# Kernel tuning notes

Measured on AMD Instinct MI355X. Metric: run time of the kernel, lower is better.

Reference implementation:

```python
import jax, jax.numpy as jnp
import numpy as np

B, T, N, D = 4, 24, 5000, 64
M, K = 256, 20
TEMP = 0.5
MASK_T = int(T * 0.2)


def _random_walk(A):
    # D^-1 A with inf -> 0, as in calculate_random_walk_matrix
    deg = A.sum(axis=1)
    d_inv = jnp.where(deg > 0, 1.0 / deg, 0.0)
    return d_inv[:, None] * A


def _gnn(h, S1, S2, W, b):
    # SpatialConvOrderK, order=1, support_len=2, include_self=True
    # h: [B, C, N, T]; diffusion along node axis; 1x1 conv == channel matmul
    m1 = jnp.einsum('bcnt,mn->bcmt', h, S1)
    m2 = jnp.einsum('bcnt,mn->bcmt', h, S2)
    hc = jnp.concatenate([h, m1, m2], axis=1)  # [B, 3C, N, T]
    return jnp.einsum('bcnt,cd->bdnt', hc, W) + b[None, :, None, None]


def _encode(x, S1, S2, W_start, b_start, W1, b1, W2, b2):
    h = x @ W_start + b_start                 # [B, T, N, D]
    h = jnp.transpose(h, (0, 3, 2, 1))        # [B, D, N, T]
    h = jax.nn.relu(_gnn(h, S1, S2, W1, b1))
    h = _gnn(h, S1, S2, W2, b2)
    return h                                  # [B, D, N, T]


def _normalize(z):
    # cosine-similarity normalization over channel axis (dim=1), torch eps=1e-8
    n = jnp.sqrt(jnp.sum(z * z, axis=1, keepdims=True))
    return z / jnp.maximum(n, 1e-8)


def _forward(x, adj, W_start, b_start, W1, b1, W2, b2, Wf1, bf1, Wf2, bf2,
             missing_idx, pos_idx, neg_idx):
    S1 = _random_walk(adj)
    S2 = _random_walk(adj.T)
    h_ori = _encode(x, S1, S2, W_start, b_start, W1, b1, W2, b2)
    # augmented view: time-masked input through the same encoder
    x_aug = x.at[:, :MASK_T].set(0.0)
    h_aug = _encode(x_aug, S1, S2, W_start, b_start, W1, b1, W2, b2)
    # imputation head: final_linear1 -> relu -> final_linear2
    ht = jnp.transpose(h_ori, (0, 3, 2, 1))   # [B, T, N, D]
    y = jax.nn.relu(ht @ Wf1 + bf1) @ Wf2 + bf2  # [B, T, N, 1]
    # vectorized RSCL: batched gather + cosine sim + InfoNCE (label 0 = positive)
    Zo = _normalize(jnp.transpose(h_ori, (0, 1, 3, 2)))  # [B, D, T, N]
    Za = _normalize(jnp.transpose(h_aug, (0, 1, 3, 2)))
    anchor = Zo[..., missing_idx]             # [B, D, T, M]
    pos = Za[..., pos_idx]                    # [B, D, T, M]
    neg = Za[..., neg_idx]                    # [B, D, T, M, K]
    pos_sim = jnp.sum(anchor * pos, axis=1)                  # [B, T, M]
    neg_sim = jnp.einsum('bdtm,bdtmk->btmk', anchor, neg)    # [B, T, M, K]
    logits = jnp.concatenate([pos_sim[..., None], neg_sim], axis=-1) / TEMP
    # cross-entropy with label 0 == logsumexp - positive logit
    loss = jnp.mean(jax.nn.logsumexp(logits, axis=-1) - logits[..., 0])
    return y, loss


def setup_inputs() -> dict:
    key = jax.random.key(0)
    ks = jax.random.split(key, 12)
    x = jax.random.normal(ks[0], (B, T, N, 1), jnp.float32)
    adj = jax.random.uniform(ks[1], (N, N), jnp.float32)
    missing_idx = jax.random.randint(ks[2], (M,), 0, N)
    pos_idx = jax.random.randint(ks[3], (M,), 0, N)
    neg_idx = jax.random.randint(ks[4], (M, K), 0, N)
    s = lambda k, shp, fan: (jax.random.normal(k, shp, jnp.float32) / np.sqrt(fan)).astype(jnp.float32)
    W_start = s(ks[5], (1, D), 1.0)
    b_start = jnp.zeros((D,), jnp.float32)
    W1 = s(ks[6], (3 * D, D), 3.0 * D)
    b1 = jnp.zeros((D,), jnp.float32)
    W2 = s(ks[7], (3 * D, D), 3.0 * D)
    b2 = jnp.zeros((D,), jnp.float32)
    Wf1 = s(ks[8], (D, D // 2), float(D))
    bf1 = jnp.zeros((D // 2,), jnp.float32)
    Wf2 = s(ks[9], (D // 2, 1), float(D // 2))
    bf2 = jnp.zeros((1,), jnp.float32)
    return dict(x=x, adj=adj, W_start=W_start, b_start=b_start, W1=W1, b1=b1,
                W2=W2, b2=b2, Wf1=Wf1, bf1=bf1, Wf2=Wf2, bf2=bf2,
                missing_idx=missing_idx, pos_idx=pos_idx, neg_idx=neg_idx)


def reference(x, adj, W_start, b_start, W1, b1, W2, b2, Wf1, bf1, Wf2, bf2,
              missing_idx, pos_idx, neg_idx):
    return _forward(x, adj, W_start, b_start, W1, b1, W2, b2, Wf1, bf1, Wf2, bf2,
                    missing_idx, pos_idx, neg_idx)
```

## Files before the change

kernel.cpp:

```cpp
#include <hip/hip_runtime.h>

typedef unsigned char u8;
typedef unsigned short u16;
typedef unsigned int u32;
typedef __attribute__((ext_vector_type(8))) short short8;
typedef __attribute__((ext_vector_type(8))) u16 u16x8;
typedef __attribute__((ext_vector_type(4))) float f32x4;
typedef __attribute__((ext_vector_type(4))) int i32x4;
typedef __attribute__((ext_vector_type(8))) int i32x8;

#define N_NODES 5000
#define NP 5120
#define BTOT 96
#define J_DIM 6144
#define TT 24
#define KNEG 20

__device__ __forceinline__ float b2f(u16 u){ union{u32 i; float f;} x; x.i = ((u32)u)<<16; return x.f; }
__device__ __forceinline__ u16 f2b(float f){ union{float fl; u32 i;} x; x.fl = f; u32 r = (x.i + 0x7fffu + ((x.i>>16)&1u))>>16; return (u16)r; }
__device__ __forceinline__ u8 f2e4(float f){ return (u8)(__builtin_amdgcn_cvt_pk_fp8_f32(f, 0.f, 0, false) & 0xff); }

#define GPERM(r) ((((r)>>1)&3) | (((r)&1)<<2))
#define GLOAD16(g, l) __builtin_amdgcn_global_load_lds((const __attribute__((address_space(1))) void*)(g), (__attribute__((address_space(3))) void*)(l), 16, 0, 0)

__global__ void k_prep(const float* __restrict__ Ws, const float* __restrict__ bs,
                       const float* __restrict__ W1, const float* __restrict__ b1,
                       const float* __restrict__ W2, float* __restrict__ consts,
                       u16* __restrict__ w2t)
{
  int d = threadIdx.x;
  float u0=0.f,u1=0.f,u2=0.f,bb=0.f;
  for (int c=0;c<64;c++){
    float w = Ws[c];
    float a = W1[c*64+d], b_ = W1[(64+c)*64+d], cw = W1[(128+c)*64+d];
    u0 += w*a; u1 += w*b_; u2 += w*cw;
    bb += bs[c]*(a+b_+cw);
  }
  bb += b1[d];
  consts[d]=u0; consts[64+d]=u1; consts[128+d]=u2; consts[192+d]=bb;
  __shared__ float rb[64];
  rb[d] = fmaxf(bb, 0.f);
  __syncthreads();
  float cA=0.f,cB=0.f,cC=0.f;
  for (int c=0;c<64;c++){
    float r = rb[c];
    cA += r*W2[c*64+d]; cB += r*W2[(64+c)*64+d]; cC += r*W2[(128+c)*64+d];
  }
  consts[256+d]=cA; consts[320+d]=cB; consts[384+d]=cC;
  for (int c=0;c<192;c++) w2t[d*192 + c] = f2b(W2[c*64 + d]);
}

__global__ __launch_bounds__(256) void k_convT(const float* __restrict__ adj,
    u8* __restrict__ abf, u8* __restrict__ atbf,
    float* __restrict__ degr, float* __restrict__ degc)
{
  __shared__ u8 tN[64][80];
  __shared__ u8 tT[64][80];
  __shared__ float rsum[64], csum[64];
  const int tid = threadIdx.x;
  const int bx = blockIdx.x, by = blockIdx.y;
  if (tid < 64){ rsum[tid] = 0.f; csum[tid] = 0.f; }
  __syncthreads();
  const int c4 = (tid & 15) * 4;
  const int r0 = tid >> 4;
  const int gk = bx*64 + c4;
  float ca0=0.f, ca1=0.f, ca2=0.f, ca3=0.f;
  #pragma unroll
  for (int p=0;p<4;p++){
    int r = p*16 + r0;
    int gm = by*64 + r;
    float v0=0.f,v1=0.f,v2=0.f,v3=0.f;
    if (gm < N_NODES && gk + 3 < N_NODES){
      const float4 v = *(const float4*)(adj + (size_t)gm*N_NODES + gk);
      v0=v.x; v1=v.y; v2=v.z; v3=v.w;
    }
    u8 p0=f2e4(v0), p1=f2e4(v1), p2=f2e4(v2), p3=f2e4(v3);
    *(u32*)&tN[r][c4] = (u32)p0 | ((u32)p1<<8) | ((u32)p2<<16) | ((u32)p3<<24);
    tT[c4+0][r]=p0; tT[c4+1][r]=p1; tT[c4+2][r]=p2; tT[c4+3][r]=p3;
    float ls = v0+v1+v2+v3;
    if (ls != 0.f) atomicAdd(&rsum[r], ls);
    ca0+=v0; ca1+=v1; ca2+=v2; ca3+=v3;
  }
  atomicAdd(&csum[c4+0], ca0); atomicAdd(&csum[c4+1], ca1);
  atomicAdd(&csum[c4+2], ca2); atomicAdd(&csum[c4+3], ca3);
  __syncthreads();
  if (tid < 64){
    int gm = by*64 + tid;
    if (gm < N_NODES && rsum[tid] != 0.f) atomicAdd(&degr[gm], rsum[tid]);
    int gc = bx*64 + tid;
    if (gc < N_NODES && csum[tid] != 0.f) atomicAdd(&degc[gc], csum[tid]);
  }
  const int j = tid >> 2, c16 = (tid & 3) * 16;
  *(i32x4*)(abf  + (size_t)(by*64+j)*NP + bx*64 + c16) = *(const i32x4*)(&tN[j][c16]);
  *(i32x4*)(atbf + (size_t)(bx*64+j)*NP + by*64 + c16) = *(const i32x4*)(&tT[j][c16]);
}

__global__ void k_xbf(const float* __restrict__ x, u8* __restrict__ xbf){
  int i4 = (blockIdx.x*256 + threadIdx.x)*4;
  int j = i4 / NP, n = i4 - j*NP;
  u32 w = 0;
  if (j < BTOT){
    #pragma unroll
    for (int e=0;e<4;e++){
      float v = (n+e < N_NODES) ? x[(size_t)j*N_NODES + n + e] : 0.f;
      w |= ((u32)f2e4(v)) << (8*e);
    }
  }
  *(u32*)(xbf + i4) = w;
}

__device__ __forceinline__ i32x8 frag8(const u8* lds, int row, int kb2){
  int g = GPERM(row & 7);
  int ba = row*128 + ((kb2 ^ g)<<4);
  union { i32x8 v; i32x4 h[2]; } f;
  f.h[0] = *(const i32x4*)(lds + ba);
  f.h[1] = *(const i32x4*)(lds + (ba^16));
  return f.v;
}

__global__ __launch_bounds__(256) void k_sgemm8(const u8* __restrict__ abf,
    const u8* __restrict__ atbf, const u8* __restrict__ B,
    float* __restrict__ y1sl, float* __restrict__ y2sl)
{
  __shared__ __align__(16) u8 lA[128*128];
  __shared__ __align__(16) u8 lB[128*128];
  const u8* A = blockIdx.z ? atbf : abf;
  float* ysl = blockIdx.z ? y2sl : y1sl;
  const int tid = threadIdx.x, lane = tid & 63, wv = tid >> 6;
  const int wm = (wv >> 1) * 64, wj = (wv & 1) * 64;
  const int m0 = blockIdx.x * 128;
  const int kbase = blockIdx.y * 640;
  f32x4 acc[4][4] = {};
  const int q = tid >> 3;
  const int sc = ((tid & 7) ^ GPERM(q & 7)) << 4;
  const u8* gA = A + (size_t)(m0 + q)*NP + kbase + sc;
  const u8* gB = B + (size_t)q*NP + kbase + sc;
  for (int k0 = 0; k0 < 640; k0 += 128) {
    #pragma unroll
    for (int s=0;s<4;s++){
      GLOAD16(gA + (size_t)(s*32)*NP + k0, (char*)lA + s*4096 + wv*1024);
      GLOAD16(gB + (size_t)(s*32)*NP + k0, (char*)lB + s*4096 + wv*1024);
    }
    __syncthreads();
    i32x8 af[4], bfv[4];
    const int kb2 = (lane >> 4) * 2;
    #pragma unroll
    for (int i=0;i<4;i++){
      af[i]  = frag8(lA, wm + i*16 + (lane&15), kb2);
      bfv[i] = frag8(lB, wj + i*16 + (lane&15), kb2);
    }
    #pragma unroll
    for (int i=0;i<4;i++)
      #pragma unroll
      for (int j=0;j<4;j++)
        acc[i][j] = __builtin_amdgcn_mfma_scale_f32_16x16x128_f8f6f4(
            af[i], bfv[j], acc[i][j], 0, 0, 0, 0x7f7f7f7f, 0, 0x7f7f7f7f);
    __syncthreads();
  }
  float* yb = ysl + (size_t)blockIdx.y * NP * 128;
  #pragma unroll
  for (int i=0;i<4;i++)
    #pragma unroll
    for (int r=0;r<4;r++){
      int row = m0 + wm + i*16 + (lane>>4)*4 + r;
      #pragma unroll
      for (int j=0;j<4;j++){
        int col = wj + j*16 + (lane&15);
        yb[(size_t)row*128 + col] = acc[i][j][r];
      }
    }
}

__global__ __launch_bounds__(256) void k_yred(const float* __restrict__ y1sl,
    const float* __restrict__ y2sl, const float* __restrict__ degr,
    const float* __restrict__ degc, float* __restrict__ y1r, float* __restrict__ y2r)
{
  __shared__ float tb[128][66];
  const int n0 = blockIdx.x*64;
  const int bt = threadIdx.x & 127, nh = threadIdx.x >> 7;
  const int nl = threadIdx.x & 63, bh = threadIdx.x >> 6;
  #pragma unroll 4
  for (int k=0;k<32;k++){
    int n = nh*32 + k;
    float s = 0.f;
    #pragma unroll
    for (int sl=0; sl<8; sl++) s += y1sl[((size_t)sl*NP + n0+n)*128 + bt];
    tb[bt][n] = s;
  }
  __syncthreads();
  {
    float dv = degr[n0+nl];
    float iv = (dv > 0.f) ? 1.f/dv : 0.f;
    #pragma unroll 4
    for (int b=0;b<32;b++){
      int btw = bh*32 + b;
      y1r[(size_t)btw*NP + n0 + nl] = iv * tb[btw][nl];
    }
  }
  __syncthreads();
  #pragma unroll 4
  for (int k=0;k<32;k++){
    int n = nh*32 + k;
    float s = 0.f;
    #pragma unroll
    for (int sl=0; sl<8; sl++) s += y2sl[((size_t)sl*NP + n0+n)*128 + bt];
    tb[bt][n] = s;
  }
  __syncthreads();
  {
    float dv = degc[n0+nl];
    float iv = (dv > 0.f) ? 1.f/dv : 0.f;
    #pragma unroll 4
    for (int b=0;b<32;b++){
      int btw = bh*32 + b;
      y2r[(size_t)btw*NP + n0 + nl] = iv * tb[btw][nl];
    }
  }
}

__global__ __launch_bounds__(256) void k_h1(const float* __restrict__ x,
    const float* __restrict__ y1r, const float* __restrict__ y2r,
    const float* __restrict__ consts, u8* __restrict__ h1t, u16* __restrict__ h1n)
{
  __shared__ u8 trT[64][80];
  const int tid = threadIdx.x;
  const int n = tid & 63, d0 = (tid >> 6) * 16;
  const int n0 = blockIdx.x * 64;
  const int bt = blockIdx.y;
  const int gn = n0 + n;
  const bool valid = gn < N_NODES;
  float xv  = valid ? x[(size_t)bt*N_NODES + gn] : 0.f;
  float y1s = y1r[(size_t)bt*NP + gn];
  float y2s = y2r[(size_t)bt*NP + gn];
  float hv[16];
  #pragma unroll
  for (int e=0;e<16;e++){
    int d = d0 + e;
    float v = 0.f;
    if (valid)
      v = fmaxf(xv*consts[d] + y1s*consts[64+d] + y2s*consts[128+d] + consts[192+d], 0.f);
    hv[e] = v;
    trT[d][n] = f2e4(v);
  }
  u16x8 p0, p1;
  #pragma unroll
  for (int e=0;e<8;e++){ p0[e]=f2b(hv[e]); p1[e]=f2b(hv[8+e]); }
  u16* dst = h1n + (size_t)gn*J_DIM + bt*64 + d0;
  *(u16x8*)dst = p0;
  *(u16x8*)(dst+8) = p1;
  __syncthreads();
  const int d = tid >> 2, c16 = (tid & 3) * 16;
  *(i32x4*)(h1t + (size_t)(bt*64+d)*NP + n0 + c16) = *(const i32x4*)(&trT[d][c16]);
}

__global__ __launch_bounds__(256) void k_gemm8(
    const u8* __restrict__ abf, const u8* __restrict__ atbf,
    const u8* __restrict__ Bt, u16* __restrict__ Pb, u16* __restrict__ Qb,
    const float* __restrict__ degr, const float* __restrict__ degc)
{
  __shared__ __align__(16) u8 lA[128*128];
  __shared__ __align__(16) u8 lB[128*128];
  const u8* A = blockIdx.z ? atbf : abf;
  u16* C = blockIdx.z ? Qb : Pb;
  const float* dg = blockIdx.z ? degc : degr;
  const int tid = threadIdx.x, lane = tid & 63, wv = tid >> 6;
  const int wm = (wv >> 1) * 64, wj = (wv & 1) * 64;
  const int m0 = blockIdx.x * 128;
  const int j0 = blockIdx.y * 128;
  f32x4 acc[4][4] = {};
  const int q = tid >> 3;
  const int sc = ((tid & 7) ^ GPERM(q & 7)) << 4;
  const u8* gA = A + (size_t)(m0 + q)*NP + sc;
  const u8* gB = Bt + (size_t)(j0 + q)*NP + sc;
  for (int k0 = 0; k0 < NP; k0 += 128) {
    #pragma unroll
    for (int s=0;s<4;s++){
      GLOAD16(gA + (size_t)(s*32)*NP + k0, (char*)lA + s*4096 + wv*1024);
      GLOAD16(gB + (size_t)(s*32)*NP + k0, (char*)lB + s*4096 + wv*1024);
    }
    __syncthreads();
    i32x8 af[4], bfv[4];
    const int kb2 = (lane >> 4) * 2;
    #pragma unroll
    for (int i=0;i<4;i++){
      af[i]  = frag8(lA, wm + i*16 + (lane&15), kb2);
      bfv[i] = frag8(lB, wj + i*16 + (lane&15), kb2);
    }
    #pragma unroll
    for (int i=0;i<4;i++)
      #pragma unroll
      for (int j=0;j<4;j++)
        acc[i][j] = __builtin_amdgcn_mfma_scale_f32_16x16x128_f8f6f4(
            af[i], bfv[j], acc[i][j], 0, 0, 0, 0x7f7f7f7f, 0, 0x7f7f7f7f);
    __syncthreads();
  }
  #pragma unroll
  for (int i=0;i<4;i++)
    #pragma unroll
    for (int r=0;r<4;r++){
      int row = m0 + wm + i*16 + (lane>>4)*4 + r;
      float dv = dg[row];
      float scl = (dv > 0.f) ? 1.f/dv : 0.f;
      #pragma unroll
      for (int j=0;j<4;j++){
        int col = j0 + wj + j*16 + (lane&15);
        C[(size_t)row*J_DIM + col] = f2b(acc[i][j][r] * scl);
      }
    }
}

__global__ __launch_bounds__(256) void k_comb(const u16* __restrict__ h1n,
  const u16* __restrict__ P, const u16* __restrict__ Q,
  const u16* __restrict__ w2t, const float* __restrict__ b2,
  const float* __restrict__ Wf1, const float* __restrict__ bf1,
  const float* __restrict__ Wf2, const float* __restrict__ bf2,
  u16* __restrict__ hori, float* __restrict__ yout)
{
  __shared__ float w1L[64*33];
  __shared__ float hT[64][65];
  __shared__ float b1L[32], w2Ls[32];
  const int tid = threadIdx.x;
  for (int i = tid; i < 2048; i += 256) w1L[(i>>5)*33 + (i&31)] = Wf1[i];
  if (tid < 32){ b1L[tid] = bf1[tid]; w2Ls[tid] = Wf2[tid]; }
  const int lane = tid & 63;
  const int wv = tid >> 6;
  const int n0 = blockIdx.x * 64 + wv * 16;
  const int bt = blockIdx.y;
  const int rl = lane & 15, kh = lane >> 4;

  f32x4 acc[4] = {};
  const size_t rowoff = (size_t)(n0 + rl) * J_DIM + bt*64;
  const u16* bases[3] = { h1n + rowoff, P + rowoff, Q + rowoff };
  #pragma unroll
  for (int s=0;s<3;s++){
    const u16* base = bases[s];
    #pragma unroll
    for (int kk=0;kk<2;kk++){
      short8 af = *(const short8*)(base + kk*32 + kh*8);
      #pragma unroll
      for (int j=0;j<4;j++){
        short8 bf = *(const short8*)(w2t + (j*16+rl)*192 + s*64 + kk*32 + kh*8);
        acc[j] = __builtin_amdgcn_mfma_f32_16x16x32_bf16(af, bf, acc[j], 0,0,0);
      }
    }
  }
  #pragma unroll
  for (int j=0;j<4;j++){
    int d = j*16 + rl;
    float bias = b2[d];
    #pragma unroll
    for (int r=0;r<4;r++){
      float hv = acc[j][r] + bias;
      int nn = n0 + kh*4 + r;
      hT[wv*16 + kh*4 + r][d] = hv;
      if (nn < N_NODES)
        hori[((size_t)bt*N_NODES + nn)*64 + d] = f2b(hv);
    }
  }
  __syncthreads();
  const int q = tid & 3, node = tid >> 2;
  float h[16];
  #pragma unroll
  for (int e=0;e<16;e++) h[e] = hT[node][q*16 + e];
  float yacc = 0.f;
  #pragma unroll
  for (int jj=0; jj<32; jj++){
    float s = 0.f;
    #pragma unroll
    for (int dl=0; dl<16; dl++) s += h[dl]*w1L[(q*16+dl)*33 + jj];
    s += __shfl_xor(s, 1);
    s += __shfl_xor(s, 2);
    s += b1L[jj];
    yacc += fmaxf(s, 0.f)*w2Ls[jj];
  }
  int gn = blockIdx.x*64 + node;
  if (q == 0 && gn < N_NODES)
    yout[(size_t)bt*N_NODES + gn] = yacc + bf2[0];
}

__global__ __launch_bounds__(256) void k_loss(const u16* __restrict__ hori,
  const int* __restrict__ missing, const int* __restrict__ posi, const int* __restrict__ negi,
  const float* __restrict__ degr, const float* __restrict__ degc,
  const float* __restrict__ consts, const float* __restrict__ b2, float* __restrict__ out)
{
  const int lane = threadIdx.x & 63;
  const int wv = threadIdx.x >> 6;
  const int wg = blockIdx.x*4 + wv;
  const int m = wg & 255;
  const int bt = wg >> 8;
  const int t_ = bt % TT;
  const float cAv = consts[256+lane], cBv = consts[320+lane], cCv = consts[384+lane], b2v = b2[lane];

  int na = missing[m];
  float va = b2f(hori[((size_t)bt*N_NODES + na)*64 + lane]);
  float ss = va*va;
  #pragma unroll
  for (int o=32;o;o>>=1) ss += __shfl_xor(ss, o);
  va /= fmaxf(sqrtf(ss), 1e-8f);

  float l0 = 0.f, mx, se;
  {
    int node = posi[m];
    float v;
    if (t_ >= 4) v = b2f(hori[((size_t)bt*N_NODES + node)*64 + lane]);
    else {
      float r1 = (degr[node] > 0.f) ? 1.f : 0.f;
      float r2 = (degc[node] > 0.f) ? 1.f : 0.f;
      v = cAv + r1*cBv + r2*cCv + b2v;
    }
    float s2 = v*v;
    #pragma unroll
    for (int o=32;o;o>>=1) s2 += __shfl_xor(s2, o);
    v /= fmaxf(sqrtf(s2), 1e-8f);
    float dp = va*v;
    #pragma unroll
    for (int o=32;o;o>>=1) dp += __shfl_xor(dp, o);
    l0 = dp * 2.f;
  }
  mx = l0; se = 1.f;
  for (int k=0;k<KNEG;k++){
    int node = negi[m*KNEG + k];
    float v;
    if (t_ >= 4) v = b2f(hori[((size_t)bt*N_NODES + node)*64 + lane]);
    else {
      float r1 = (degr[node] > 0.f) ? 1.f : 0.f;
      float r2 = (degc[node] > 0.f) ? 1.f : 0.f;
      v = cAv + r1*cBv + r2*cCv + b2v;
    }
    float s2 = v*v;
    #pragma unroll
    for (int o=32;o;o>>=1) s2 += __shfl_xor(s2, o);
    v /= fmaxf(sqrtf(s2), 1e-8f);
    float dp = va*v;
    #pragma unroll
    for (int o=32;o;o>>=1) dp += __shfl_xor(dp, o);
    float lk = dp * 2.f;
    if (lk > mx){ se = se*expf(mx-lk) + 1.f; mx = lk; }
    else se += expf(lk-mx);
  }
  float term = logf(se) + mx - l0;
  __shared__ float red[4];
  if (lane == 0) red[wv] = term;
  __syncthreads();
  if (threadIdx.x == 0)
    atomicAdd(out + 480000, (red[0]+red[1]+red[2]+red[3]) * (1.f/24576.f));
}

extern "C" void kernel_launch(void* const* d_in, const int* in_sizes, int n_in,
                              void* d_out, int out_size, void* d_ws, size_t ws_size,
                              hipStream_t stream)
{
  const float* x   = (const float*)d_in[0];
  const float* adj = (const float*)d_in[1];
  const float* Ws  = (const float*)d_in[2];
  const float* bs  = (const float*)d_in[3];
  const float* W1  = (const float*)d_in[4];
  const float* b1  = (const float*)d_in[5];
  const float* W2  = (const float*)d_in[6];
  const float* b2  = (const float*)d_in[7];
  const float* Wf1 = (const float*)d_in[8];
  const float* bf1 = (const float*)d_in[9];
  const float* Wf2 = (const float*)d_in[10];
  const float* bf2 = (const float*)d_in[11];
  const int* missing = (const int*)d_in[12];
  const int* posi    = (const int*)d_in[13];
  const int* negi    = (const int*)d_in[14];
  float* out = (float*)d_out;

  char* w = (char*)d_ws;
  u8*  abf   = (u8*) (w + 0);
  u8*  atbf  = (u8*) (w + 26214400);
  u8*  h1t   = (u8*) (w + 52428800);
  u16* h1n   = (u16*)(w + 83886080);
  u16* Pb    = (u16*)(w + 146800640);
  u16* Qb    = (u16*)(w + 209715200);
  u8*  xbf   = (u8*) (w + 272629760);
  float* degr = (float*)(w + 273285120);
  float* degc = (float*)(w + 273305600);
  float* consts = (float*)(w + 273326080);
  u16* w2t   = (u16*)(w + 273328128);
  u16*   hori  = (u16*)(w + 0);
  float* y1sl  = (float*)(w + 146800640);
  float* y2sl  = (float*)(w + 167772160);
  float* y1r   = (float*)(w + 209715200);
  float* y2r   = (float*)(w + 212336640);

  hipMemsetAsync(degr, 0, 40960, stream);
  hipMemsetAsync(out + 480000, 0, 4, stream);

  k_prep<<<1, 64, 0, stream>>>(Ws, bs, W1, b1, W2, consts, w2t);
  k_convT<<<dim3(80,80), 256, 0, stream>>>(adj, abf, atbf, degr, degc);
  k_xbf<<<640, 256, 0, stream>>>(x, xbf);
  k_sgemm8<<<dim3(40,8,2), 256, 0, stream>>>(abf, atbf, xbf, y1sl, y2sl);
  k_yred<<<80, 256, 0, stream>>>(y1sl, y2sl, degr, degc, y1r, y2r);
  k_h1<<<dim3(80,96), 256, 0, stream>>>(x, y1r, y2r, consts, h1t, h1n);
  k_gemm8<<<dim3(40,48,2), 256, 0, stream>>>(abf, atbf, h1t, Pb, Qb, degr, degc);
  k_comb<<<dim3(80,96), 256, 0, stream>>>(h1n, Pb, Qb, w2t, b2, Wf1, bf1, Wf2, bf2, hori, out);
  k_loss<<<6144, 256, 0, stream>>>(hori, missing, posi, negi, degr, degc, consts, b2, out);
}
```

Measured before the change: 819.2 us.

## Pre-normalize embeddings in combine kernel and simplify loss and degree reductions

The combine kernel now L2-normalizes each node embedding before storing it. The loss kernel therefore only does dot products and no longer computes a per-gather norm. For early masked timesteps the four possible constant vectors are pre-normalized in the prep kernel. The loss uses unrolled independent gathers with a two-pass logsumexp, and the adjacency conversion replaces LDS atomics with shuffle and partial-sum reductions. Storing normalized bf16 values changes rounding slightly, and the larger unrolled loss kernel may raise register use.

```diff
diff --git a/kernel.cpp b/kernel.cpp
--- a/kernel.cpp
+++ b/kernel.cpp
@@ -25,8 +25,8 @@
 
 __global__ void k_prep(const float* __restrict__ Ws, const float* __restrict__ bs,
                        const float* __restrict__ W1, const float* __restrict__ b1,
-                       const float* __restrict__ W2, float* __restrict__ consts,
-                       u16* __restrict__ w2t)
+                       const float* __restrict__ W2, const float* __restrict__ b2,
+                       float* __restrict__ consts, u16* __restrict__ w2t)
 {
   int d = threadIdx.x;
   float u0=0.f,u1=0.f,u2=0.f,bb=0.f;
@@ -48,6 +48,17 @@
   }
   consts[256+d]=cA; consts[320+d]=cB; consts[384+d]=cC;
   for (int c=0;c<192;c++) w2t[d*192 + c] = f2b(W2[c*64 + d]);
+  __syncthreads();
+  float b2v = b2[d];
+  for (int vi=0; vi<4; vi++){
+    float vv = cA + ((vi&1) ? cB : 0.f) + ((vi&2) ? cC : 0.f) + b2v;
+    rb[d] = vv*vv;
+    __syncthreads();
+    for (int o=32;o;o>>=1){ if (d<o) rb[d]+=rb[d+o]; __syncthreads(); }
+    float nrm = sqrtf(rb[0]);
+    consts[448 + vi*64 + d] = vv / fmaxf(nrm, 1e-8f);
+    __syncthreads();
+  }
 }
 
 __global__ __launch_bounds__(256) void k_convT(const float* __restrict__ adj,
@@ -56,18 +67,17 @@
 {
   __shared__ u8 tN[64][80];
   __shared__ u8 tT[64][80];
-  __shared__ float rsum[64], csum[64];
+  __shared__ float rsum[64];
+  __shared__ float cpart[16][64];
   const int tid = threadIdx.x;
   const int bx = blockIdx.x, by = blockIdx.y;
-  if (tid < 64){ rsum[tid] = 0.f; csum[tid] = 0.f; }
-  __syncthreads();
   const int c4 = (tid & 15) * 4;
-  const int r0 = tid >> 4;
+  const int g  = tid >> 4;
   const int gk = bx*64 + c4;
   float ca0=0.f, ca1=0.f, ca2=0.f, ca3=0.f;
   #pragma unroll
   for (int p=0;p<4;p++){
-    int r = p*16 + r0;
+    int r = p*16 + g;
     int gm = by*64 + r;
     float v0=0.f,v1=0.f,v2=0.f,v3=0.f;
     if (gm < N_NODES && gk + 3 < N_NODES){
@@ -78,17 +88,21 @@
     *(u32*)&tN[r][c4] = (u32)p0 | ((u32)p1<<8) | ((u32)p2<<16) | ((u32)p3<<24);
     tT[c4+0][r]=p0; tT[c4+1][r]=p1; tT[c4+2][r]=p2; tT[c4+3][r]=p3;
     float ls = v0+v1+v2+v3;
-    if (ls != 0.f) atomicAdd(&rsum[r], ls);
+    ls += __shfl_xor(ls,1); ls += __shfl_xor(ls,2);
+    ls += __shfl_xor(ls,4); ls += __shfl_xor(ls,8);
+    if ((tid & 15) == 0) rsum[r] = ls;
     ca0+=v0; ca1+=v1; ca2+=v2; ca3+=v3;
   }
-  atomicAdd(&csum[c4+0], ca0); atomicAdd(&csum[c4+1], ca1);
-  atomicAdd(&csum[c4+2], ca2); atomicAdd(&csum[c4+3], ca3);
+  cpart[g][c4+0]=ca0; cpart[g][c4+1]=ca1; cpart[g][c4+2]=ca2; cpart[g][c4+3]=ca3;
   __syncthreads();
   if (tid < 64){
     int gm = by*64 + tid;
     if (gm < N_NODES && rsum[tid] != 0.f) atomicAdd(&degr[gm], rsum[tid]);
+    float cs = 0.f;
+    #pragma unroll
+    for (int gg=0;gg<16;gg++) cs += cpart[gg][tid];
     int gc = bx*64 + tid;
-    if (gc < N_NODES && csum[tid] != 0.f) atomicAdd(&degc[gc], csum[tid]);
+    if (gc < N_NODES && cs != 0.f) atomicAdd(&degc[gc], cs);
   }
   const int j = tid >> 2, c16 = (tid & 3) * 16;
   *(i32x4*)(abf  + (size_t)(by*64+j)*NP + bx*64 + c16) = *(const i32x4*)(&tN[j][c16]);
@@ -314,7 +328,7 @@
   const u16* __restrict__ w2t, const float* __restrict__ b2,
   const float* __restrict__ Wf1, const float* __restrict__ bf1,
   const float* __restrict__ Wf2, const float* __restrict__ bf2,
-  u16* __restrict__ hori, float* __restrict__ yout)
+  u16* __restrict__ horin, float* __restrict__ yout)
 {
   __shared__ float w1L[64*33];
   __shared__ float hT[64][65];
@@ -344,17 +358,31 @@
       }
     }
   }
+  float hvv[4][4];
+  #pragma unroll
+  for (int j=0;j<4;j++){
+    float bias = b2[j*16 + rl];
+    #pragma unroll
+    for (int r=0;r<4;r++) hvv[j][r] = acc[j][r] + bias;
+  }
+  float inv[4];
+  #pragma unroll
+  for (int r=0;r<4;r++){
+    float s = hvv[0][r]*hvv[0][r] + hvv[1][r]*hvv[1][r]
+            + hvv[2][r]*hvv[2][r] + hvv[3][r]*hvv[3][r];
+    s += __shfl_xor(s,1); s += __shfl_xor(s,2);
+    s += __shfl_xor(s,4); s += __shfl_xor(s,8);
+    inv[r] = 1.f / fmaxf(sqrtf(s), 1e-8f);
+  }
   #pragma unroll
   for (int j=0;j<4;j++){
     int d = j*16 + rl;
-    float bias = b2[d];
     #pragma unroll
     for (int r=0;r<4;r++){
-      float hv = acc[j][r] + bias;
       int nn = n0 + kh*4 + r;
-      hT[wv*16 + kh*4 + r][d] = hv;
+      hT[wv*16 + kh*4 + r][d] = hvv[j][r];
       if (nn < N_NODES)
-        hori[((size_t)bt*N_NODES + nn)*64 + d] = f2b(hv);
+        horin[((size_t)bt*N_NODES + nn)*64 + d] = f2b(hvv[j][r] * inv[r]);
     }
   }
   __syncthreads();
@@ -378,67 +406,43 @@
     yout[(size_t)bt*N_NODES + gn] = yacc + bf2[0];
 }
 
-__global__ __launch_bounds__(256) void k_loss(const u16* __restrict__ hori,
+__global__ __launch_bounds__(256) void k_loss(const u16* __restrict__ horin,
   const int* __restrict__ missing, const int* __restrict__ posi, const int* __restrict__ negi,
   const float* __restrict__ degr, const float* __restrict__ degc,
-  const float* __restrict__ consts, const float* __restrict__ b2, float* __restrict__ out)
+  const float* __restrict__ consts, float* __restrict__ out)
 {
   const int lane = threadIdx.x & 63;
   const int wv = threadIdx.x >> 6;
   const int wg = blockIdx.x*4 + wv;
   const int m = wg & 255;
   const int bt = wg >> 8;
-  const int t_ = bt % TT;
-  const float cAv = consts[256+lane], cBv = consts[320+lane], cCv = consts[384+lane], b2v = b2[lane];
+  const bool early = (bt % TT) < 4;
 
   int na = missing[m];
-  float va = b2f(hori[((size_t)bt*N_NODES + na)*64 + lane]);
-  float ss = va*va;
-  #pragma unroll
-  for (int o=32;o;o>>=1) ss += __shfl_xor(ss, o);
-  va /= fmaxf(sqrtf(ss), 1e-8f);
-
-  float l0 = 0.f, mx, se;
-  {
-    int node = posi[m];
+  float va = b2f(horin[((size_t)bt*N_NODES + na)*64 + lane]);
+
+  float lk[KNEG+1];
+  #pragma unroll
+  for (int k=0;k<=KNEG;k++){
+    int node = (k==0) ? posi[m] : negi[m*KNEG + (k-1)];
     float v;
-    if (t_ >= 4) v = b2f(hori[((size_t)bt*N_NODES + node)*64 + lane]);
+    if (!early) v = b2f(horin[((size_t)bt*N_NODES + node)*64 + lane]);
     else {
-      float r1 = (degr[node] > 0.f) ? 1.f : 0.f;
-      float r2 = (degc[node] > 0.f) ? 1.f : 0.f;
-      v = cAv + r1*cBv + r2*cCv + b2v;
-    }
-    float s2 = v*v;
-    #pragma unroll
-    for (int o=32;o;o>>=1) s2 += __shfl_xor(s2, o);
-    v /= fmaxf(sqrtf(s2), 1e-8f);
+      int vi = (degr[node] > 0.f ? 1 : 0) + (degc[node] > 0.f ? 2 : 0);
+      v = consts[448 + vi*64 + lane];
+    }
     float dp = va*v;
     #pragma unroll
     for (int o=32;o;o>>=1) dp += __shfl_xor(dp, o);
-    l0 = dp * 2.f;
-  }
-  mx = l0; se = 1.f;
-  for (int k=0;k<KNEG;k++){
-    int node = negi[m*KNEG + k];
-    float v;
-    if (t_ >= 4) v = b2f(hori[((size_t)bt*N_NODES + node)*64 + lane]);
-    else {
-      float r1 = (degr[node] > 0.f) ? 1.f : 0.f;
-      float r2 = (degc[node] > 0.f) ? 1.f : 0.f;
-      v = cAv + r1*cBv + r2*cCv + b2v;
-    }
-    float s2 = v*v;
-    #pragma unroll
-    for (int o=32;o;o>>=1) s2 += __shfl_xor(s2, o);
-    v /= fmaxf(sqrtf(s2), 1e-8f);
-    float dp = va*v;
-    #pragma unroll
-    for (int o=32;o;o>>=1) dp += __shfl_xor(dp, o);
-    float lk = dp * 2.f;
-    if (lk > mx){ se = se*expf(mx-lk) + 1.f; mx = lk; }
-    else se += expf(lk-mx);
-  }
-  float term = logf(se) + mx - l0;
+    lk[k] = dp * 2.f;
+  }
+  float mx = lk[0];
+  #pragma unroll
+  for (int k=1;k<=KNEG;k++) mx = fmaxf(mx, lk[k]);
+  float se = 0.f;
+  #pragma unroll
+  for (int k=0;k<=KNEG;k++) se += expf(lk[k]-mx);
+  float term = logf(se) + mx - lk[0];
   __shared__ float red[4];
   if (lane == 0) red[wv] = term;
   __syncthreads();
@@ -478,8 +482,8 @@
   float* degr = (float*)(w + 273285120);
   float* degc = (float*)(w + 273305600);
   float* consts = (float*)(w + 273326080);
-  u16* w2t   = (u16*)(w + 273328128);
-  u16*   hori  = (u16*)(w + 0);
+  u16* w2t   = (u16*)(w + 273330176);
+  u16*   horin = (u16*)(w + 0);
   float* y1sl  = (float*)(w + 146800640);
   float* y2sl  = (float*)(w + 167772160);
   float* y1r   = (float*)(w + 209715200);
@@ -488,13 +492,13 @@
   hipMemsetAsync(degr, 0, 40960, stream);
   hipMemsetAsync(out + 480000, 0, 4, stream);
 
-  k_prep<<<1, 64, 0, stream>>>(Ws, bs, W1, b1, W2, consts, w2t);
+  k_prep<<<1, 64, 0, stream>>>(Ws, bs, W1, b1, W2, b2, consts, w2t);
   k_convT<<<dim3(80,80), 256, 0, stream>>>(adj, abf, atbf, degr, degc);
   k_xbf<<<640, 256, 0, stream>>>(x, xbf);
   k_sgemm8<<<dim3(40,8,2), 256, 0, stream>>>(abf, atbf, xbf, y1sl, y2sl);
   k_yred<<<80, 256, 0, stream>>>(y1sl, y2sl, degr, degc, y1r, y2r);
   k_h1<<<dim3(80,96), 256, 0, stream>>>(x, y1r, y2r, consts, h1t, h1n);
   k_gemm8<<<dim3(40,48,2), 256, 0, stream>>>(abf, atbf, h1t, Pb, Qb, degr, degc);
-  k_comb<<<dim3(80,96), 256, 0, stream>>>(h1n, Pb, Qb, w2t, b2, Wf1, bf1, Wf2, bf2, hori, out);
-  k_loss<<<6144, 256, 0, stream>>>(hori, missing, posi, negi, degr, degc, consts, b2, out);
-}
+  k_comb<<<dim3(80,96), 256, 0, stream>>>(h1n, Pb, Qb, w2t, b2, Wf1, bf1, Wf2, bf2, horin, out);
+  k_loss<<<6144, 256, 0, stream>>>(horin, missing, posi, negi, degr, degc, consts, out);
+}
```

Result: faster. 734.4 us (-10.4%).
